# Kernel tuning notes

Measured on AMD Instinct MI355X. Metric: run time of the kernel, lower is better.

Reference implementation:

```python
import jax, jax.numpy as jnp
import numpy as np

B, S, D, H = 4, 1024, 1024, 16
DH = D // H  # head dim = 64
NEG = 1e9  # keras Softmax masking constant for fp32


def setup_inputs() -> dict:
    key = jax.random.key(0)
    ks = jax.random.split(key, 7)
    return {
        "inputs": jax.random.normal(ks[0], (B, S, D), jnp.float32),
        "mask": jax.random.randint(ks[1], (B, 1, 1, S), 0, 2) > 0,
        "interaction": jax.random.normal(ks[2], (B, S, S, H), jnp.float32) * 0.1,
        "W_Q": jax.random.normal(ks[3], (D, D), jnp.float32) * 0.02,
        "W_K": jax.random.normal(ks[4], (D, D), jnp.float32) * 0.02,
        "W_V": jax.random.normal(ks[5], (D, D), jnp.float32) * 0.02,
        "W_O": jax.random.normal(ks[6], (D, D), jnp.float32) * 0.02,
    }


def reference(inputs, mask, interaction, W_Q, W_K, W_V, W_O):
    b, s, d = inputs.shape
    def proj(W):
        # [B,S,D] @ [D,D] -> [B,S,H,DH] -> [B,H,S,DH]
        return (inputs @ W).reshape(b, s, H, DH).transpose(0, 2, 1, 3)
    Q, K, V = proj(W_Q), proj(W_K), proj(W_V)
    scores = jnp.einsum("bhqd,bhkd->bhqk", Q, K) / (DH ** 0.5)
    # interaction [B,S,S,H] -> [B,H,S,S], additive bias before softmax
    scores = scores + interaction.transpose(0, 3, 1, 2)
    # keras Softmax(mask=...): add -1e9 where mask is False, softmax over last axis
    scores = jnp.where(mask, scores, scores - NEG)
    attn = jax.nn.softmax(scores, axis=-1)
    hidden = jnp.einsum("bhqk,bhkd->bhqd", attn, V)
    hidden = hidden.transpose(0, 2, 1, 3).reshape(b, s, d)
    return hidden @ W_O
```

## Files before the change

### kernel.cpp

```cpp
#include <hip/hip_runtime.h>
#include <hip/hip_bf16.h>
#include <stdint.h>

#define BDIM 4
#define SDIM 1024
#define DDIM 1024
#define HDIM 16
#define DHDIM 64

typedef __bf16 bf16_t;
typedef __bf16 bf16x8 __attribute__((ext_vector_type(8)));
typedef __bf16 bf16x4 __attribute__((ext_vector_type(4)));
typedef float f32x4 __attribute__((ext_vector_type(4)));

typedef __attribute__((address_space(3))) uint32_t lds_u32;
typedef const __attribute__((address_space(1))) uint32_t glb_u32;

__device__ __forceinline__ void glds16(const void* g, void* l) {
    __builtin_amdgcn_global_load_lds((glb_u32*)g, (lds_u32*)l, 16, 0, 0);
}


__global__ __launch_bounds__(256) void convert_x_kernel(const float* __restrict__ X,
                                                        bf16_t* __restrict__ Xb, int n) {
    int i = (blockIdx.x * 256 + threadIdx.x) * 4;
    if (i >= n) return;
    float4 v = *(const float4*)(X + i);
    bf16x4 o;
    o[0] = (bf16_t)v.x; o[1] = (bf16_t)v.y; o[2] = (bf16_t)v.z; o[3] = (bf16_t)v.w;
    *(bf16x4*)(Xb + i) = o;
}

__global__ __launch_bounds__(256) void transpose_w_kernel(const float* __restrict__ W0,
                                                          const float* __restrict__ W1,
                                                          const float* __restrict__ W2,
                                                          const float* __restrict__ W3,
                                                          bf16_t* __restrict__ Wt) {
    __shared__ float tile[32][33];
    int z = blockIdx.z;
    const float* W = (z == 0) ? W0 : (z == 1) ? W1 : (z == 2) ? W2 : W3;
    bf16_t* dst = Wt + (size_t)z * DDIM * DDIM;
    int bx = blockIdx.x * 32;
    int by = blockIdx.y * 32;
    int x = threadIdx.x & 31, y0 = threadIdx.x >> 5;
#pragma unroll
    for (int i = 0; i < 4; i++) {
        int y = y0 + i * 8;
        tile[y][x] = W[(size_t)(by + y) * DDIM + bx + x];
    }
    __syncthreads();
#pragma unroll
    for (int i = 0; i < 4; i++) {
        int y = y0 + i * 8;
        dst[(size_t)(bx + y) * DDIM + by + x] = (bf16_t)tile[x][y];
    }
}

__global__ __launch_bounds__(1024) void mask_flag_kernel(const unsigned char* __restrict__ mb,
                                                         int* __restrict__ flag) {
    __shared__ int any;
    if (threadIdx.x == 0) any = 0;
    __syncthreads();
    int loc = 0;
    for (int i = threadIdx.x; i < BDIM * SDIM; i += 1024)
        if ((i & 3) && mb[i]) loc = 1;
    if (loc) any = 1;
    __syncthreads();
    if (threadIdx.x == 0) *flag = any ? 1 : 0;
}

template <int MODE>
__global__ __launch_bounds__(256) void gemm_bt_kernel(const bf16_t* __restrict__ A,
                                                      const bf16_t* __restrict__ Bt,
                                                      bf16_t* __restrict__ Qo, bf16_t* __restrict__ Ko,
                                                      bf16_t* __restrict__ Vto, float* __restrict__ Co) {
    __shared__ bf16_t As[128 * 32];
    __shared__ bf16_t Bs[128 * 32];
    const int m0 = blockIdx.x * 128;
    const int n0 = blockIdx.y * 128;
    const int t = threadIdx.x;
    const int lane = t & 63, w = t >> 6;
    const int wm = w & 1, wn = w >> 1;
    const int low = lane & 15, quad = lane >> 4;
    f32x4 acc[4][4] = {};

    const int srow = w * 16 + (lane >> 2);
    const int koff = (lane & 3) * 8;
    const bf16_t* Ag = A + (size_t)(m0 + srow) * DDIM + koff;
    const bf16_t* Bg = Bt + (size_t)(n0 + srow) * DDIM + koff;
    bf16_t* AsW = As + w * 512;
    bf16_t* BsW = Bs + w * 512;

    for (int k0 = 0; k0 < DDIM; k0 += 32) {
        __syncthreads();
        glds16(Ag + k0, AsW);
        glds16(Ag + (size_t)64 * DDIM + k0, AsW + 64 * 32);
        glds16(Bg + k0, BsW);
        glds16(Bg + (size_t)64 * DDIM + k0, BsW + 64 * 32);
        __syncthreads();
        bf16x8 af[4], bv[4];
#pragma unroll
        for (int mt = 0; mt < 4; mt++)
            af[mt] = *(const bf16x8*)(As + (wm * 64 + mt * 16 + low) * 32 + quad * 8);
#pragma unroll
        for (int nt = 0; nt < 4; nt++)
            bv[nt] = *(const bf16x8*)(Bs + (wn * 64 + nt * 16 + low) * 32 + quad * 8);
#pragma unroll
        for (int mt = 0; mt < 4; mt++)
#pragma unroll
            for (int nt = 0; nt < 4; nt++)
                acc[mt][nt] = __builtin_amdgcn_mfma_f32_16x16x32_bf16(af[mt], bv[nt], acc[mt][nt], 0, 0, 0);
    }

#pragma unroll
    for (int mt = 0; mt < 4; mt++) {
        const int mbase = m0 + wm * 64 + mt * 16 + quad * 4;
#pragma unroll
        for (int nt = 0; nt < 4; nt++) {
            const int ncol = n0 + wn * 64 + nt * 16 + low;
            if (MODE == 0) {
                const int which = ncol >> 10, nl = ncol & 1023;
                const int hh = nl >> 6, dh = nl & 63;
                const int bb = mbase >> 10, s = mbase & 1023;
                if (which == 2) {
                    bf16x4 pv;
#pragma unroll
                    for (int r = 0; r < 4; r++) pv[r] = (bf16_t)acc[mt][nt][r];
                    *(bf16x4*)(Vto + ((size_t)((bb * HDIM + hh) * DHDIM + dh)) * SDIM + s) = pv;
                } else if (which == 0) {
#pragma unroll
                    for (int r = 0; r < 4; r++)
                        Qo[((size_t)(bb * HDIM + hh) * SDIM + (s + r)) * DHDIM + dh] =
                            (bf16_t)(acc[mt][nt][r] * 0.125f);
                } else {
#pragma unroll
                    for (int r = 0; r < 4; r++)
                        Ko[((size_t)(bb * HDIM + hh) * SDIM + (s + r)) * DHDIM + dh] =
                            (bf16_t)acc[mt][nt][r];
                }
            } else {
#pragma unroll
                for (int r = 0; r < 4; r++)
                    Co[(size_t)(mbase + r) * DDIM + ncol] = acc[mt][nt][r];
            }
        }
    }
}

__global__ __launch_bounds__(512, 4) void attn_kernel(const bf16_t* __restrict__ Q,
                                                      const bf16_t* __restrict__ K,
                                                      const bf16_t* __restrict__ Vt,
                                                      const float* __restrict__ inter,
                                                      const unsigned char* __restrict__ maskb,
                                                      const int* __restrict__ flagp,
                                                      bf16_t* __restrict__ hid) {
    constexpr int KS = 40;
    constexpr int HS = 16 * KS + 8;
    __shared__ bf16_t bias_l[2][8 * HS];
    __shared__ bf16_t P[8][16 * KS];
    const int bid = blockIdx.x;
    const int xcd = bid & 7;
    const int b = xcd >> 1, hh = xcd & 1;
    const int q0 = (bid >> 3) * 16;
    const int t = threadIdx.x;
    const int w = t >> 6, lane = t & 63;
    const int low = lane & 15, quad = lane >> 4;
    const int h = hh * 8 + w;
    const int mstride = (*flagp) ? 1 : 4;

    const int sk = lane >> 1, shp = lane & 1;
    const float* srcB = inter + ((size_t)(b * SDIM + q0) * SDIM + sk) * HDIM + hh * 8 + shp * 4;
    const unsigned char* mb = maskb + (size_t)b * SDIM * mstride;
    constexpr size_t ROWSTRIDE = (size_t)SDIM * HDIM;

    const bf16_t* Qb = Q + ((size_t)(b * HDIM + h) * SDIM + q0) * DHDIM;
    bf16x8 qf0 = *(const bf16x8*)(Qb + low * DHDIM + quad * 8);
    bf16x8 qf1 = *(const bf16x8*)(Qb + low * DHDIM + 32 + quad * 8);

    const bf16_t* Kb = K + (size_t)(b * HDIM + h) * SDIM * DHDIM;
    const bf16_t* VtB = Vt + (size_t)(b * HDIM + h) * DHDIM * SDIM;
    bf16_t* Pw = &P[w][0];

    float mrow = -3.0e38f, lrow = 0.f;
    f32x4 accO[4] = {};

    {
        float4 v0 = *(const float4*)(srcB + (size_t)w * ROWSTRIDE);
        float4 v1 = *(const float4*)(srcB + (size_t)(w + 8) * ROWSTRIDE);
        float pen = mb[sk * mstride] ? 0.f : 1.0e9f;
        bf16_t* d0 = &bias_l[0][(shp * 4) * HS + w * KS + sk];
        bf16_t* d1 = &bias_l[0][(shp * 4) * HS + (w + 8) * KS + sk];
        d0[0 * HS] = (bf16_t)(v0.x - pen); d0[1 * HS] = (bf16_t)(v0.y - pen);
        d0[2 * HS] = (bf16_t)(v0.z - pen); d0[3 * HS] = (bf16_t)(v0.w - pen);
        d1[0 * HS] = (bf16_t)(v1.x - pen); d1[1 * HS] = (bf16_t)(v1.y - pen);
        d1[2 * HS] = (bf16_t)(v1.z - pen); d1[3 * HS] = (bf16_t)(v1.w - pen);
    }

    for (int c = 0; c < SDIM / 32; c++) {
        __syncthreads();
        const int kbase = c * 32;

        const bf16_t* kpA = Kb + (size_t)(kbase + low) * DHDIM;
        const bf16_t* kpB = Kb + (size_t)(kbase + 16 + low) * DHDIM;
        bf16x8 kA0 = *(const bf16x8*)(kpA + quad * 8);
        bf16x8 kA1 = *(const bf16x8*)(kpA + 32 + quad * 8);
        bf16x8 kB0 = *(const bf16x8*)(kpB + quad * 8);
        bf16x8 kB1 = *(const bf16x8*)(kpB + 32 + quad * 8);

        bf16x8 vf[4];
#pragma unroll
        for (int nt = 0; nt < 4; nt++)
            vf[nt] = *(const bf16x8*)(VtB + (size_t)(nt * 16 + low) * SDIM + kbase + quad * 8);

        float4 nv0, nv1; float npen = 0.f;
        if (c < SDIM / 32 - 1) {
            const float* s2 = srcB + (size_t)(c + 1) * 32 * HDIM;
            nv0 = *(const float4*)(s2 + (size_t)w * ROWSTRIDE);
            nv1 = *(const float4*)(s2 + (size_t)(w + 8) * ROWSTRIDE);
            npen = mb[((c + 1) * 32 + sk) * mstride] ? 0.f : 1.0e9f;
        }

        f32x4 s0 = {}, s1 = {};
        s0 = __builtin_amdgcn_mfma_f32_16x16x32_bf16(kA0, qf0, s0, 0, 0, 0);
        s0 = __builtin_amdgcn_mfma_f32_16x16x32_bf16(kA1, qf1, s0, 0, 0, 0);
        s1 = __builtin_amdgcn_mfma_f32_16x16x32_bf16(kB0, qf0, s1, 0, 0, 0);
        s1 = __builtin_amdgcn_mfma_f32_16x16x32_bf16(kB1, qf1, s1, 0, 0, 0);

        const bf16_t* bc = &bias_l[c & 1][w * HS + low * KS];
        bf16x4 bv0 = *(const bf16x4*)(bc + quad * 4);
        bf16x4 bv1 = *(const bf16x4*)(bc + 16 + quad * 4);
        float sv[8];
#pragma unroll
        for (int r = 0; r < 4; r++) {
            sv[r] = s0[r] + (float)bv0[r];
            sv[4 + r] = s1[r] + (float)bv1[r];
        }

        float vmx = fmaxf(fmaxf(fmaxf(sv[0], sv[1]), fmaxf(sv[2], sv[3])),
                          fmaxf(fmaxf(sv[4], sv[5]), fmaxf(sv[6], sv[7])));
        vmx = fmaxf(vmx, __shfl_xor(vmx, 16));
        vmx = fmaxf(vmx, __shfl_xor(vmx, 32));
        if (__any(vmx > mrow + 8.f)) {
            float mn = fmaxf(mrow, vmx);
            float alpha = __expf(mrow - mn);
            mrow = mn;
            lrow *= alpha;
#pragma unroll
            for (int r = 0; r < 4; r++) {
                float ar = __shfl(alpha, (lane & 48) | (quad * 4 + r));
#pragma unroll
                for (int nt = 0; nt < 4; nt++) accO[nt][r] *= ar;
            }
        }
        float e[8];
#pragma unroll
        for (int j = 0; j < 8; j++) e[j] = __expf(sv[j] - mrow);
        bf16x4 p0, p1;
#pragma unroll
        for (int j = 0; j < 4; j++) { p0[j] = (bf16_t)e[j]; p1[j] = (bf16_t)e[4 + j]; }
        float ps = ((e[0] + e[1]) + (e[2] + e[3])) + ((e[4] + e[5]) + (e[6] + e[7]));
        ps += __shfl_xor(ps, 16);
        ps += __shfl_xor(ps, 32);
        lrow += ps;

        *(bf16x4*)(Pw + low * KS + quad * 4) = p0;
        *(bf16x4*)(Pw + low * KS + 16 + quad * 4) = p1;
        bf16x8 pf = *(const bf16x8*)(Pw + low * KS + quad * 8);

#pragma unroll
        for (int nt = 0; nt < 4; nt++)
            accO[nt] = __builtin_amdgcn_mfma_f32_16x16x32_bf16(pf, vf[nt], accO[nt], 0, 0, 0);

        if (c < SDIM / 32 - 1) {
            bf16_t* d0 = &bias_l[(c + 1) & 1][(shp * 4) * HS + w * KS + sk];
            bf16_t* d1 = &bias_l[(c + 1) & 1][(shp * 4) * HS + (w + 8) * KS + sk];
            d0[0 * HS] = (bf16_t)(nv0.x - npen); d0[1 * HS] = (bf16_t)(nv0.y - npen);
            d0[2 * HS] = (bf16_t)(nv0.z - npen); d0[3 * HS] = (bf16_t)(nv0.w - npen);
            d1[0 * HS] = (bf16_t)(nv1.x - npen); d1[1 * HS] = (bf16_t)(nv1.y - npen);
            d1[2 * HS] = (bf16_t)(nv1.z - npen); d1[3 * HS] = (bf16_t)(nv1.w - npen);
        }
    }

    float linv = 1.f / lrow;
#pragma unroll
    for (int r = 0; r < 4; r++) {
        float lr = __shfl(linv, (lane & 48) | (quad * 4 + r));
#pragma unroll
        for (int nt = 0; nt < 4; nt++) {
            hid[((size_t)b * SDIM + q0 + quad * 4 + r) * DDIM + h * 64 + nt * 16 + low] =
                (bf16_t)(accO[nt][r] * lr);
        }
    }
}


extern "C" void kernel_launch(void* const* d_in, const int* in_sizes, int n_in,
                              void* d_out, int out_size, void* d_ws, size_t ws_size,
                              hipStream_t stream) {
    const float* X = (const float*)d_in[0];
    const unsigned char* maskb = (const unsigned char*)d_in[1];
    const float* inter = (const float*)d_in[2];
    const float* WQ = (const float*)d_in[3];
    const float* WK = (const float*)d_in[4];
    const float* WV = (const float*)d_in[5];
    const float* WO = (const float*)d_in[6];
    float* out = (float*)d_out;

    char* ws = (char*)d_ws;
    const size_t MB = 1024 * 1024;
    bf16_t* Xb  = (bf16_t*)(ws + 0 * MB);
    bf16_t* Wt  = (bf16_t*)(ws + 8 * MB);
    bf16_t* Qm  = (bf16_t*)(ws + 16 * MB);
    bf16_t* Km  = (bf16_t*)(ws + 24 * MB);
    bf16_t* Vtm = (bf16_t*)(ws + 32 * MB);
    bf16_t* hid = (bf16_t*)(ws + 40 * MB);
    int* flag   = (int*)(ws + 48 * MB);

    convert_x_kernel<<<BDIM * SDIM * DDIM / (256 * 4), 256, 0, stream>>>(X, Xb, BDIM * SDIM * DDIM);
    transpose_w_kernel<<<dim3(32, 32, 4), 256, 0, stream>>>(WQ, WK, WV, WO, Wt);
    mask_flag_kernel<<<1, 1024, 0, stream>>>(maskb, flag);
    gemm_bt_kernel<0><<<dim3(32, 24), 256, 0, stream>>>(Xb, Wt, Qm, Km, Vtm, nullptr);
    attn_kernel<<<dim3(512), 512, 0, stream>>>(Qm, Km, Vtm, inter, maskb, flag, hid);
    gemm_bt_kernel<1><<<dim3(32, 8), 256, 0, stream>>>(hid, Wt + (size_t)3 * DDIM * DDIM,
                                                       nullptr, nullptr, nullptr, out);
}
```

Before: 550.1 us.

## Pre-transpose masked interaction bias to bf16 and stage K/V in LDS

Adds a separate kernel that reads the fp32 interaction tensor once, applies the mask penalty, and writes a bf16 bias in [B,H,S,S] layout. The attention kernel can then load contiguous bias rows per head directly. The attention kernel is also remapped so each block handles one (batch, head) with 128 queries across 8 waves. K and V tiles are staged into swizzled, double-buffered LDS via global_load_lds and shared by all waves. This trades an extra 128MB bf16 write plus read of the bias for coalesced access and K/V reuse across waves, and it raises workspace use to beyond 64MB.

```diff
diff --git a/kernel.cpp b/kernel.cpp
--- a/kernel.cpp
+++ b/kernel.cpp
@@ -67,6 +67,41 @@
     if (loc) any = 1;
     __syncthreads();
     if (threadIdx.x == 0) *flag = any ? 1 : 0;
+}
+
+__global__ __launch_bounds__(256) void transpose_bias_kernel(const float* __restrict__ inter,
+                                                             const unsigned char* __restrict__ maskb,
+                                                             const int* __restrict__ flagp,
+                                                             bf16_t* __restrict__ biasT) {
+    __shared__ bf16_t tile[16 * 8 * 136];
+    const int k0 = blockIdx.x * 128, q0 = blockIdx.y * 8, b = blockIdx.z;
+    const int tid = threadIdx.x;
+    const int mstride = (*flagp) ? 1 : 4;
+    const unsigned char* mb = maskb + (size_t)b * SDIM * mstride;
+    const float* src = inter + ((size_t)(b * SDIM + q0) * SDIM + k0) * HDIM;
+#pragma unroll
+    for (int it = 0; it < 16; it++) {
+        int j = it * 256 + tid;
+        int h4 = j & 3, k = (j >> 2) & 127, q = j >> 9;
+        float4 v = *(const float4*)(src + ((size_t)q * SDIM + k) * HDIM + h4 * 4);
+        float pen = mb[(k0 + k) * mstride] ? 0.f : 1.0e9f;
+        bf16_t* d = &tile[(h4 * 4) * 1088 + q * 136 + k];
+        d[0 * 1088] = (bf16_t)(v.x - pen);
+        d[1 * 1088] = (bf16_t)(v.y - pen);
+        d[2 * 1088] = (bf16_t)(v.z - pen);
+        d[3 * 1088] = (bf16_t)(v.w - pen);
+    }
+    __syncthreads();
+#pragma unroll
+    for (int rep = 0; rep < 2; rep++) {
+        int u = rep * 256 + tid;
+        int h = u >> 5, q = (u >> 2) & 7, kp = u & 3;
+        const bf16_t* s = &tile[h * 1088 + q * 136 + kp * 32];
+        bf16_t* d = biasT + ((size_t)(b * HDIM + h) * SDIM + (q0 + q)) * SDIM + k0 + kp * 32;
+#pragma unroll
+        for (int ss = 0; ss < 4; ss++)
+            *(bf16x8*)(d + ss * 8) = *(const bf16x8*)(s + ss * 8);
+    }
 }
 
 template <int MODE>
@@ -150,75 +185,74 @@
 __global__ __launch_bounds__(512, 4) void attn_kernel(const bf16_t* __restrict__ Q,
                                                       const bf16_t* __restrict__ K,
                                                       const bf16_t* __restrict__ Vt,
-                                                      const float* __restrict__ inter,
-                                                      const unsigned char* __restrict__ maskb,
-                                                      const int* __restrict__ flagp,
+                                                      const bf16_t* __restrict__ biasT,
                                                       bf16_t* __restrict__ hid) {
-    constexpr int KS = 40;
-    constexpr int HS = 16 * KS + 8;
-    __shared__ bf16_t bias_l[2][8 * HS];
-    __shared__ bf16_t P[8][16 * KS];
+    __shared__ bf16_t Ks[2][2048];
+    __shared__ bf16_t Vs[2][2048];
+    __shared__ bf16_t P[8][16 * 40];
     const int bid = blockIdx.x;
-    const int xcd = bid & 7;
-    const int b = xcd >> 1, hh = xcd & 1;
-    const int q0 = (bid >> 3) * 16;
+    const int b = bid & 3, h = (bid >> 2) & 15, qg = bid >> 6;
+    const int q0 = qg * 128;
     const int t = threadIdx.x;
     const int w = t >> 6, lane = t & 63;
     const int low = lane & 15, quad = lane >> 4;
-    const int h = hh * 8 + w;
-    const int mstride = (*flagp) ? 1 : 4;
-
-    const int sk = lane >> 1, shp = lane & 1;
-    const float* srcB = inter + ((size_t)(b * SDIM + q0) * SDIM + sk) * HDIM + hh * 8 + shp * 4;
-    const unsigned char* mb = maskb + (size_t)b * SDIM * mstride;
-    constexpr size_t ROWSTRIDE = (size_t)SDIM * HDIM;
-
-    const bf16_t* Qb = Q + ((size_t)(b * HDIM + h) * SDIM + q0) * DHDIM;
+    const int qw = q0 + w * 16;
+
+    const bf16_t* Qb = Q + ((size_t)(b * HDIM + h) * SDIM + qw) * DHDIM;
     bf16x8 qf0 = *(const bf16x8*)(Qb + low * DHDIM + quad * 8);
     bf16x8 qf1 = *(const bf16x8*)(Qb + low * DHDIM + 32 + quad * 8);
 
     const bf16_t* Kb = K + (size_t)(b * HDIM + h) * SDIM * DHDIM;
     const bf16_t* VtB = Vt + (size_t)(b * HDIM + h) * DHDIM * SDIM;
+    const bf16_t* Bq = biasT + ((size_t)(b * HDIM + h) * SDIM + qw + low) * SDIM;
     bf16_t* Pw = &P[w][0];
+
+    const bf16_t* stg_src;
+    size_t kmul;
+    bf16_t* stg_base;
+    if (w < 4) {
+        int rl = lane >> 3, us = lane & 7;
+        stg_src = Kb + (size_t)(w * 8 + rl) * DHDIM + (us ^ rl) * 8;
+        kmul = DHDIM;
+        stg_base = &Ks[0][0] + w * 512;
+    } else {
+        int dl = lane >> 2, ks = lane & 3;
+        stg_src = VtB + (size_t)((w - 4) * 16 + dl) * SDIM + (ks ^ (dl & 3)) * 8;
+        kmul = 1;
+        stg_base = &Vs[0][0] + (w - 4) * 512;
+    }
 
     float mrow = -3.0e38f, lrow = 0.f;
     f32x4 accO[4] = {};
 
-    {
-        float4 v0 = *(const float4*)(srcB + (size_t)w * ROWSTRIDE);
-        float4 v1 = *(const float4*)(srcB + (size_t)(w + 8) * ROWSTRIDE);
-        float pen = mb[sk * mstride] ? 0.f : 1.0e9f;
-        bf16_t* d0 = &bias_l[0][(shp * 4) * HS + w * KS + sk];
-        bf16_t* d1 = &bias_l[0][(shp * 4) * HS + (w + 8) * KS + sk];
-        d0[0 * HS] = (bf16_t)(v0.x - pen); d0[1 * HS] = (bf16_t)(v0.y - pen);
-        d0[2 * HS] = (bf16_t)(v0.z - pen); d0[3 * HS] = (bf16_t)(v0.w - pen);
-        d1[0 * HS] = (bf16_t)(v1.x - pen); d1[1 * HS] = (bf16_t)(v1.y - pen);
-        d1[2 * HS] = (bf16_t)(v1.z - pen); d1[3 * HS] = (bf16_t)(v1.w - pen);
-    }
+    glds16(stg_src, stg_base);
+    bf16x4 bv0 = *(const bf16x4*)(Bq + quad * 4);
+    bf16x4 bv1 = *(const bf16x4*)(Bq + 16 + quad * 4);
 
     for (int c = 0; c < SDIM / 32; c++) {
         __syncthreads();
         const int kbase = c * 32;
 
-        const bf16_t* kpA = Kb + (size_t)(kbase + low) * DHDIM;
-        const bf16_t* kpB = Kb + (size_t)(kbase + 16 + low) * DHDIM;
-        bf16x8 kA0 = *(const bf16x8*)(kpA + quad * 8);
-        bf16x8 kA1 = *(const bf16x8*)(kpA + 32 + quad * 8);
-        bf16x8 kB0 = *(const bf16x8*)(kpB + quad * 8);
-        bf16x8 kB1 = *(const bf16x8*)(kpB + 32 + quad * 8);
-
+        bf16x4 nb0 = bv0, nb1 = bv1;
+        if (c < SDIM / 32 - 1) {
+            glds16(stg_src + (size_t)(kbase + 32) * kmul, stg_base + ((c + 1) & 1) * 2048);
+            nb0 = *(const bf16x4*)(Bq + kbase + 32 + quad * 4);
+            nb1 = *(const bf16x4*)(Bq + kbase + 48 + quad * 4);
+        }
+
+        const bf16_t* Kl = &Ks[c & 1][0];
+        const int sw7 = low & 7;
+        bf16x8 kA0 = *(const bf16x8*)(Kl + low * 64 + (quad ^ sw7) * 8);
+        bf16x8 kA1 = *(const bf16x8*)(Kl + low * 64 + ((quad + 4) ^ sw7) * 8);
+        bf16x8 kB0 = *(const bf16x8*)(Kl + (16 + low) * 64 + (quad ^ sw7) * 8);
+        bf16x8 kB1 = *(const bf16x8*)(Kl + (16 + low) * 64 + ((quad + 4) ^ sw7) * 8);
+
+        const bf16_t* Vl = &Vs[c & 1][0];
+        const int sw3 = low & 3;
         bf16x8 vf[4];
 #pragma unroll
         for (int nt = 0; nt < 4; nt++)
-            vf[nt] = *(const bf16x8*)(VtB + (size_t)(nt * 16 + low) * SDIM + kbase + quad * 8);
-
-        float4 nv0, nv1; float npen = 0.f;
-        if (c < SDIM / 32 - 1) {
-            const float* s2 = srcB + (size_t)(c + 1) * 32 * HDIM;
-            nv0 = *(const float4*)(s2 + (size_t)w * ROWSTRIDE);
-            nv1 = *(const float4*)(s2 + (size_t)(w + 8) * ROWSTRIDE);
-            npen = mb[((c + 1) * 32 + sk) * mstride] ? 0.f : 1.0e9f;
-        }
+            vf[nt] = *(const bf16x8*)(Vl + (nt * 16 + low) * 32 + (quad ^ sw3) * 8);
 
         f32x4 s0 = {}, s1 = {};
         s0 = __builtin_amdgcn_mfma_f32_16x16x32_bf16(kA0, qf0, s0, 0, 0, 0);
@@ -226,9 +260,6 @@
         s1 = __builtin_amdgcn_mfma_f32_16x16x32_bf16(kB0, qf0, s1, 0, 0, 0);
         s1 = __builtin_amdgcn_mfma_f32_16x16x32_bf16(kB1, qf1, s1, 0, 0, 0);
 
-        const bf16_t* bc = &bias_l[c & 1][w * HS + low * KS];
-        bf16x4 bv0 = *(const bf16x4*)(bc + quad * 4);
-        bf16x4 bv1 = *(const bf16x4*)(bc + 16 + quad * 4);
         float sv[8];
 #pragma unroll
         for (int r = 0; r < 4; r++) {
@@ -263,22 +294,15 @@
         ps += __shfl_xor(ps, 32);
         lrow += ps;
 
-        *(bf16x4*)(Pw + low * KS + quad * 4) = p0;
-        *(bf16x4*)(Pw + low * KS + 16 + quad * 4) = p1;
-        bf16x8 pf = *(const bf16x8*)(Pw + low * KS + quad * 8);
+        *(bf16x4*)(Pw + low * 40 + quad * 4) = p0;
+        *(bf16x4*)(Pw + low * 40 + 16 + quad * 4) = p1;
+        bf16x8 pf = *(const bf16x8*)(Pw + low * 40 + quad * 8);
 
 #pragma unroll
         for (int nt = 0; nt < 4; nt++)
             accO[nt] = __builtin_amdgcn_mfma_f32_16x16x32_bf16(pf, vf[nt], accO[nt], 0, 0, 0);
 
-        if (c < SDIM / 32 - 1) {
-            bf16_t* d0 = &bias_l[(c + 1) & 1][(shp * 4) * HS + w * KS + sk];
-            bf16_t* d1 = &bias_l[(c + 1) & 1][(shp * 4) * HS + (w + 8) * KS + sk];
-            d0[0 * HS] = (bf16_t)(nv0.x - npen); d0[1 * HS] = (bf16_t)(nv0.y - npen);
-            d0[2 * HS] = (bf16_t)(nv0.z - npen); d0[3 * HS] = (bf16_t)(nv0.w - npen);
-            d1[0 * HS] = (bf16_t)(nv1.x - npen); d1[1 * HS] = (bf16_t)(nv1.y - npen);
-            d1[2 * HS] = (bf16_t)(nv1.z - npen); d1[3 * HS] = (bf16_t)(nv1.w - npen);
-        }
+        bv0 = nb0; bv1 = nb1;
     }
 
     float linv = 1.f / lrow;
@@ -287,7 +311,7 @@
         float lr = __shfl(linv, (lane & 48) | (quad * 4 + r));
 #pragma unroll
         for (int nt = 0; nt < 4; nt++) {
-            hid[((size_t)b * SDIM + q0 + quad * 4 + r) * DDIM + h * 64 + nt * 16 + low] =
+            hid[((size_t)b * SDIM + qw + quad * 4 + r) * DDIM + h * 64 + nt * 16 + low] =
                 (bf16_t)(accO[nt][r] * lr);
         }
     }
@@ -308,19 +332,21 @@
 
     char* ws = (char*)d_ws;
     const size_t MB = 1024 * 1024;
-    bf16_t* Xb  = (bf16_t*)(ws + 0 * MB);
-    bf16_t* Wt  = (bf16_t*)(ws + 8 * MB);
-    bf16_t* Qm  = (bf16_t*)(ws + 16 * MB);
-    bf16_t* Km  = (bf16_t*)(ws + 24 * MB);
-    bf16_t* Vtm = (bf16_t*)(ws + 32 * MB);
-    bf16_t* hid = (bf16_t*)(ws + 40 * MB);
-    int* flag   = (int*)(ws + 48 * MB);
+    bf16_t* Xb    = (bf16_t*)(ws + 0 * MB);
+    bf16_t* Wt    = (bf16_t*)(ws + 8 * MB);
+    bf16_t* Qm    = (bf16_t*)(ws + 16 * MB);
+    bf16_t* Km    = (bf16_t*)(ws + 24 * MB);
+    bf16_t* Vtm   = (bf16_t*)(ws + 32 * MB);
+    bf16_t* hid   = (bf16_t*)(ws + 40 * MB);
+    int* flag     = (int*)(ws + 48 * MB);
+    bf16_t* biasT = (bf16_t*)(ws + 64 * MB);
 
     convert_x_kernel<<<BDIM * SDIM * DDIM / (256 * 4), 256, 0, stream>>>(X, Xb, BDIM * SDIM * DDIM);
     transpose_w_kernel<<<dim3(32, 32, 4), 256, 0, stream>>>(WQ, WK, WV, WO, Wt);
     mask_flag_kernel<<<1, 1024, 0, stream>>>(maskb, flag);
+    transpose_bias_kernel<<<dim3(8, 128, 4), 256, 0, stream>>>(inter, maskb, flag, biasT);
     gemm_bt_kernel<0><<<dim3(32, 24), 256, 0, stream>>>(Xb, Wt, Qm, Km, Vtm, nullptr);
-    attn_kernel<<<dim3(512), 512, 0, stream>>>(Qm, Km, Vtm, inter, maskb, flag, hid);
+    attn_kernel<<<dim3(512), 512, 0, stream>>>(Qm, Km, Vtm, biasT, hid);
     gemm_bt_kernel<1><<<dim3(32, 8), 256, 0, stream>>>(hid, Wt + (size_t)3 * DDIM * DDIM,
                                                        nullptr, nullptr, nullptr, out);
 }
```

Result: faster. 536.7 us (-2.4%).
